# Kernel optimization log

Measured on AMD Instinct MI355X. Metric: run time of the kernel, lower is better.

Reference implementation:

```python
import jax, jax.numpy as jnp
import numpy as np

B, N, E, D = 32, 512, 2048, 128
N_STEPS = 3


def setup_inputs() -> dict:
    key = jax.random.key(0)
    ks = jax.random.split(key, 16)
    s = 0.05
    return {
        "prop_state": jax.random.normal(ks[0], (B, N, D), jnp.float32),
        "edge_states": jax.random.normal(ks[1], (B, E, D), jnp.float32),
        "A": jax.random.uniform(ks[2], (B, N, E), jnp.float32) / E,
        "tem_features": jax.random.normal(ks[3], (B, 64), jnp.float32),
        "link_W": jax.random.normal(ks[4], (D, D), jnp.float32) * s,
        "link_b": jnp.zeros((D,), jnp.float32),
        "reset_W": jax.random.normal(ks[5], (2 * D, D), jnp.float32) * s,
        "reset_b": jnp.zeros((D,), jnp.float32),
        "update_W": jax.random.normal(ks[6], (2 * D, D), jnp.float32) * s,
        "update_b": jnp.zeros((D,), jnp.float32),
        "trans_W": jax.random.normal(ks[7], (2 * D, D), jnp.float32) * s,
        "trans_b": jnp.zeros((D,), jnp.float32),
        "att_W1": jax.random.normal(ks[8], (D, D), jnp.float32) * s,
        "att_b1": jnp.zeros((D,), jnp.float32),
        "att_W2": jax.random.normal(ks[9], (D, 1), jnp.float32) * s,
        "att_b2": jnp.zeros((1,), jnp.float32),
        "out_W": jax.random.normal(ks[10], (D, D), jnp.float32) * s,
        "out_b": jnp.zeros((D,), jnp.float32),
    }


def reference(prop_state, edge_states, A, tem_features,
              link_W, link_b, reset_W, reset_b, update_W, update_b,
              trans_W, trans_b, att_W1, att_b1, att_W2, att_b2, out_W, out_b):
    init_node = prop_state
    init_edge = edge_states
    for _ in range(N_STEPS):
        edge_states = edge_states @ link_W + link_b              # [B,E,D]
        a_cur = jnp.einsum('bne,bed->bnd', A, edge_states)       # [B,N,D]
        a = jnp.concatenate([a_cur, prop_state], axis=2)         # [B,N,2D]
        r = jax.nn.sigmoid(a @ reset_W + reset_b)
        z = jax.nn.sigmoid(a @ update_W + update_b)
        joined = jnp.concatenate([a_cur, r * prop_state], axis=2)
        h_hat = jnp.tanh(joined @ trans_W + trans_b)
        prop_state = (1.0 - z) * prop_state + z * h_hat
    # attention pooling
    atten = jnp.tanh(prop_state @ att_W1 + att_b1) @ att_W2 + att_b2   # [B,N,1]
    Aw = jax.nn.softmax(jnp.transpose(atten, (0, 2, 1)), axis=2)       # [B,1,N]
    out = jnp.tanh(prop_state @ out_W + out_b)                         # [B,N,D]
    mul = jnp.einsum('bqn,bnd->bqd', Aw, out)                          # [B,1,D]
    graph_out = jnp.tanh(jnp.squeeze(mul, axis=1))                     # [B,D]
    # residual block: mean over concatenated node+edge initial states
    feat = jnp.concatenate([init_node, init_edge], axis=1)             # [B,N+E,D]
    residual = jnp.mean(feat, axis=1)                                  # [B,D]
    res = jax.nn.relu(graph_out + residual)
    return res, mul, edge_states
```

## Files before the change

kernel.cpp:

```cpp
#include <hip/hip_runtime.h>
#include <hip/hip_bf16.h>


typedef unsigned short u16;
typedef __attribute__((ext_vector_type(4))) float f32x4;
typedef __attribute__((ext_vector_type(8))) short bf16x8;

#define DI static __device__ __forceinline__

DI u16 f2bf(float f) {
    unsigned u = __builtin_bit_cast(unsigned, f);
    return (u16)((u + 0x7fffu + ((u >> 16) & 1u)) >> 16);
}

DI bf16x8 cvt8(float4 a, float4 b) {
    u16 tmp[8] = {f2bf(a.x), f2bf(a.y), f2bf(a.z), f2bf(a.w),
                  f2bf(b.x), f2bf(b.y), f2bf(b.z), f2bf(b.w)};
    return *(const bf16x8*)tmp;
}

DI int imgIdx(int k, int n) {
    return (((k >> 5) * 128 + n) * 4 + (((k >> 3) & 3) ^ ((n >> 1) & 3))) * 8 + (k & 7);
}
DI bf16x8 wfragG(const u16* __restrict__ img, int kc, int tt, int l15, int quad) {
    return *(const bf16x8*)&img[(((kc * 128 + tt * 16 + l15) * 4) + (quad ^ ((l15 >> 1) & 3))) * 8];
}

#define MFMA16(a, b, c) __builtin_amdgcn_mfma_f32_16x16x32_bf16(a, b, c, 0, 0, 0)

__global__ __launch_bounds__(256) void k_prep1(
    const float* __restrict__ linkW, const float* __restrict__ resetW,
    const float* __restrict__ updateW, const float* __restrict__ transW,
    const float* __restrict__ attW1, const float* __restrict__ outW,
    float* __restrict__ W2, u16* __restrict__ linkImg, u16* __restrict__ WrImg,
    u16* __restrict__ WzImg, u16* __restrict__ WhImg, u16* __restrict__ attW1Img,
    u16* __restrict__ outWImg)
{
    int blk = blockIdx.x, t = threadIdx.x;
    if (blk < 256) {
        int idx = blk * 256 + t;
        int out = idx >> 2, q = idx & 3;
        int r = out >> 7, c = out & 127;
        const float* ar = linkW + r * 128 + q * 32;
        float acc = 0.f;
#pragma unroll
        for (int k = 0; k < 32; k++) acc += ar[k] * linkW[(q * 32 + k) * 128 + c];
        acc += __shfl_xor(acc, 1);
        acc += __shfl_xor(acc, 2);
        if (q == 0) W2[out] = acc;
    } else {
        const float* src; u16* dst; int base;
        if (blk < 260)      { src = resetW;  dst = WrImg;    base = 256; }
        else if (blk < 264) { src = updateW; dst = WzImg;    base = 260; }
        else if (blk < 268) { src = transW;  dst = WhImg;    base = 264; }
        else if (blk < 270) { src = linkW;   dst = linkImg;  base = 268; }
        else if (blk < 272) { src = attW1;   dst = attW1Img; base = 270; }
        else                { src = outW;    dst = outWImg;  base = 272; }
        int off = (blk - base) * 8192;
        for (int i = 0; i < 32; i++) {
            int e = off + t + i * 256;
            int k = e >> 7, n = e & 127;
            dst[imgIdx(k, n)] = f2bf(src[e]);
        }
    }
}

__global__ __launch_bounds__(256) void k_prep2(
    const float* __restrict__ linkW, const float* __restrict__ linkb,
    const float* __restrict__ W2, u16* __restrict__ W3Img, float* __restrict__ ebias)
{
    int blk = blockIdx.x, t = threadIdx.x;
    if (blk < 256) {
        int idx = blk * 256 + t;
        int out = idx >> 2, q = idx & 3;
        int r = out >> 7, c = out & 127;
        const float* ar = W2 + r * 128 + q * 32;
        float acc = 0.f;
#pragma unroll
        for (int k = 0; k < 32; k++) acc += ar[k] * linkW[(q * 32 + k) * 128 + c];
        acc += __shfl_xor(acc, 1);
        acc += __shfl_xor(acc, 2);
        if (q == 0) W3Img[imgIdx(r, c)] = f2bf(acc);
    } else if (t < 128) {
        float acc = linkb[t];
#pragma unroll 8
        for (int k = 0; k < 128; k++) acc += linkb[k] * (W2[k * 128 + t] + linkW[k * 128 + t]);
        ebias[t] = acc;
    }
}

__global__ __launch_bounds__(256) void k_te(
    const float* __restrict__ E0, u16* __restrict__ Eswz, float* __restrict__ resid)
{
    __shared__ alignas(16) u16 sT[4096];
    __shared__ float sCol[128];
    int t = threadIdx.x, kc = blockIdx.x, b = blockIdx.y;
    const float* Eb = E0 + (size_t)b * 262144 + (size_t)kc * 32 * 128;
    if (t < 128) sCol[t] = 0.f;
    float part[4] = {0.f, 0.f, 0.f, 0.f};
    int ncol = (t & 31) * 4;
    for (int i = 0; i < 4; i++) {
        int f4i = t + i * 256;
        int k5 = f4i >> 5;
        float4 v = *(const float4*)&Eb[k5 * 128 + ncol];
        int g = k5 >> 3, o = k5 & 7;
        float vv[4] = {v.x, v.y, v.z, v.w};
#pragma unroll
        for (int j = 0; j < 4; j++) {
            int n = ncol + j;
            sT[(n * 4 + (g ^ ((n >> 1) & 3))) * 8 + o] = f2bf(vv[j]);
            part[j] += vv[j];
        }
    }
    __syncthreads();
#pragma unroll
    for (int j = 0; j < 4; j++) atomicAdd(&sCol[ncol + j], part[j]);
    u16* dst = Eswz + (size_t)b * 262144 + (size_t)kc * 4096;
    ((uint4*)dst)[t] = ((const uint4*)sT)[t];
    ((uint4*)dst)[t + 256] = ((const uint4*)sT)[t + 256];
    __syncthreads();
    if (t < 128) atomicAdd(&resid[b * 128 + t], sCol[t]);
}

__global__ __launch_bounds__(256, 3) void k_g0(
    const float* __restrict__ A, const u16* __restrict__ Eswz,
    u16* __restrict__ aOut, float* __restrict__ rowsum)
{
    __shared__ float sAcc[4][16][128];
    __shared__ float sRs[4][16];
    int t = threadIdx.x, wid = t >> 6, lane = t & 63, l15 = lane & 15, quad = lane >> 4;
    int bx = blockIdx.x;
    int g = bx >> 8, rmod = bx & 255;
    int b = (rmod & 7) + 8 * g;
    int s = (rmod >> 3) & 31;
    size_t r0 = (size_t)b * 512 + (size_t)s * 16;
    const u16* Eb = Eswz + (size_t)b * 262144;
    const float* Ar = A + (r0 + l15) * 2048;
    int kbase = wid * 16;

    f32x4 acc[8];
#pragma unroll
    for (int i = 0; i < 8; i++) acc[i] = (f32x4){0.f, 0.f, 0.f, 0.f};
    float rsum = 0.f;

    float4 xc = *(const float4*)&Ar[kbase * 32 + quad * 8];
    float4 yc = *(const float4*)&Ar[kbase * 32 + quad * 8 + 4];
    bf16x8 bc[8];
#pragma unroll
    for (int tt = 0; tt < 8; tt++) bc[tt] = wfragG(Eb, kbase, tt, l15, quad);

    for (int kc = 0; kc < 16; kc++) {
        int kg = kbase + kc;
        float4 xn, yn; bf16x8 bn[8];
        if (kc < 15) {
            xn = *(const float4*)&Ar[(kg + 1) * 32 + quad * 8];
            yn = *(const float4*)&Ar[(kg + 1) * 32 + quad * 8 + 4];
#pragma unroll
            for (int tt = 0; tt < 8; tt++) bn[tt] = wfragG(Eb, kg + 1, tt, l15, quad);
        }
        rsum += xc.x + xc.y + xc.z + xc.w + yc.x + yc.y + yc.z + yc.w;
        bf16x8 af = cvt8(xc, yc);
#pragma unroll
        for (int tt = 0; tt < 8; tt++) acc[tt] = MFMA16(af, bc[tt], acc[tt]);
        if (kc < 15) {
            xc = xn; yc = yn;
#pragma unroll
            for (int tt = 0; tt < 8; tt++) bc[tt] = bn[tt];
        }
    }
    rsum += __shfl_xor(rsum, 16);
    rsum += __shfl_xor(rsum, 32);
    if (quad == 0) sRs[wid][l15] = rsum;
#pragma unroll
    for (int tt = 0; tt < 8; tt++)
#pragma unroll
        for (int r = 0; r < 4; r++)
            sAcc[wid][quad * 4 + r][tt * 16 + l15] = acc[tt][r];
    __syncthreads();
    {
        int row = t >> 4, c8 = (t & 15) * 8;
        u16 o[8];
#pragma unroll
        for (int j = 0; j < 8; j++) {
            float v = sAcc[0][row][c8 + j] + sAcc[1][row][c8 + j] +
                      sAcc[2][row][c8 + j] + sAcc[3][row][c8 + j];
            o[j] = f2bf(v);
        }
        *(uint4*)&aOut[(r0 + row) * 128 + c8] = *(const uint4*)o;
    }
    if (t < 16)
        rowsum[r0 + t] = sRs[0][t] + sRs[1][t] + sRs[2][t] + sRs[3][t];
}

__global__ __launch_bounds__(256) void k_steps(
    const u16* __restrict__ aBuf0, const float* __restrict__ p0,
    const float* __restrict__ rowsum,
    const u16* __restrict__ linkImg, const u16* __restrict__ WrImg,
    const u16* __restrict__ WzImg, const u16* __restrict__ WhImg,
    const u16* __restrict__ attW1Img, const u16* __restrict__ outWImg,
    const float* __restrict__ link_b, const float* __restrict__ reset_b,
    const float* __restrict__ update_b, const float* __restrict__ trans_b,
    const float* __restrict__ att_b1, const float* __restrict__ att_W2,
    const float* __restrict__ att_b2, const float* __restrict__ out_b,
    float* __restrict__ atten, float* __restrict__ outPool,
    float* __restrict__ resid)
{
    __shared__ alignas(16) u16 sA[16 * 136], sRP[16 * 136], sP[16 * 136];
    __shared__ float sRed[16];
    int t = threadIdx.x, wave = t >> 6, lane = t & 63, l15 = lane & 15, quad = lane >> 4;
    size_t r0 = (size_t)blockIdx.x * 16;
    int bb = blockIdx.x >> 5;
    int ttA = wave * 2, ttB = wave * 2 + 1;
    int colA = ttA * 16 + l15, colB = ttB * 16 + l15;
    if (t < 16) sRed[t] = 0.f;

    bf16x8 aF[4], pF[4];
#pragma unroll
    for (int kc = 0; kc < 4; kc++) {
        aF[kc] = *(const bf16x8*)&aBuf0[(r0 + l15) * 128 + kc * 32 + quad * 8];
        float4 x = *(const float4*)&p0[(r0 + l15) * 128 + kc * 32 + quad * 8];
        float4 y = *(const float4*)&p0[(r0 + l15) * 128 + kc * 32 + quad * 8 + 4];
        pF[kc] = cvt8(x, y);
    }
    f32x4 pS[2];
#pragma unroll
    for (int j = 0; j < 2; j++)
#pragma unroll
        for (int r = 0; r < 4; r++)
            pS[j][r] = p0[(r0 + quad * 4 + r) * 128 + (wave * 2 + j) * 16 + l15];
    {
        float s0 = pS[0][0] + pS[0][1] + pS[0][2] + pS[0][3];
        float s1 = pS[1][0] + pS[1][1] + pS[1][2] + pS[1][3];
        s0 += __shfl_xor(s0, 16); s0 += __shfl_xor(s0, 32);
        s1 += __shfl_xor(s1, 16); s1 += __shfl_xor(s1, 32);
        if (quad == 0) {
            atomicAdd(&resid[bb * 128 + colA], s0);
            atomicAdd(&resid[bb * 128 + colB], s1);
        }
    }
    float sv[4];
#pragma unroll
    for (int r = 0; r < 4; r++) sv[r] = rowsum[r0 + quad * 4 + r];
    float lbA = link_b[colA], lbB = link_b[colB];
    float rbA = reset_b[colA], rbB = reset_b[colB];
    float ubA = update_b[colA], ubB = update_b[colB];
    float tbA = trans_b[colA], tbB = trans_b[colB];

    f32x4 zero4 = {0.f, 0.f, 0.f, 0.f};
    for (int step = 0; step < 3; step++) {
        f32x4 cA = zero4, cB = zero4;
#pragma unroll
        for (int kc = 0; kc < 4; kc++) {
            cA = MFMA16(aF[kc], wfragG(linkImg, kc, ttA, l15, quad), cA);
            cB = MFMA16(aF[kc], wfragG(linkImg, kc, ttB, l15, quad), cB);
        }
#pragma unroll
        for (int r = 0; r < 4; r++) {
            sA[(quad * 4 + r) * 136 + colA] = f2bf(cA[r] + sv[r] * lbA);
            sA[(quad * 4 + r) * 136 + colB] = f2bf(cB[r] + sv[r] * lbB);
        }
        __syncthreads();
#pragma unroll
        for (int kc = 0; kc < 4; kc++)
            aF[kc] = *(const bf16x8*)&sA[l15 * 136 + kc * 32 + quad * 8];
        f32x4 rA = zero4, rB = zero4, zA = zero4, zB = zero4;
#pragma unroll
        for (int kc = 0; kc < 8; kc++) {
            bf16x8 af = (kc < 4) ? aF[kc] : pF[kc - 4];
            rA = MFMA16(af, wfragG(WrImg, kc, ttA, l15, quad), rA);
            rB = MFMA16(af, wfragG(WrImg, kc, ttB, l15, quad), rB);
            zA = MFMA16(af, wfragG(WzImg, kc, ttA, l15, quad), zA);
            zB = MFMA16(af, wfragG(WzImg, kc, ttB, l15, quad), zB);
        }
#pragma unroll
        for (int r = 0; r < 4; r++) {
            float rvA = 1.f / (1.f + __expf(-(rA[r] + rbA)));
            float rvB = 1.f / (1.f + __expf(-(rB[r] + rbB)));
            zA[r] = 1.f / (1.f + __expf(-(zA[r] + ubA)));
            zB[r] = 1.f / (1.f + __expf(-(zB[r] + ubB)));
            sRP[(quad * 4 + r) * 136 + colA] = f2bf(rvA * pS[0][r]);
            sRP[(quad * 4 + r) * 136 + colB] = f2bf(rvB * pS[1][r]);
        }
        __syncthreads();
        bf16x8 rpF[4];
#pragma unroll
        for (int kc = 0; kc < 4; kc++)
            rpF[kc] = *(const bf16x8*)&sRP[l15 * 136 + kc * 32 + quad * 8];
        f32x4 hA = zero4, hB = zero4;
#pragma unroll
        for (int kc = 0; kc < 8; kc++) {
            bf16x8 af = (kc < 4) ? aF[kc] : rpF[kc - 4];
            hA = MFMA16(af, wfragG(WhImg, kc, ttA, l15, quad), hA);
            hB = MFMA16(af, wfragG(WhImg, kc, ttB, l15, quad), hB);
        }
#pragma unroll
        for (int r = 0; r < 4; r++) {
            float h1 = tanhf(hA[r] + tbA), h2 = tanhf(hB[r] + tbB);
            pS[0][r] = (1.f - zA[r]) * pS[0][r] + zA[r] * h1;
            pS[1][r] = (1.f - zB[r]) * pS[1][r] + zB[r] * h2;
            sP[(quad * 4 + r) * 136 + colA] = f2bf(pS[0][r]);
            sP[(quad * 4 + r) * 136 + colB] = f2bf(pS[1][r]);
        }
        __syncthreads();
#pragma unroll
        for (int kc = 0; kc < 4; kc++)
            pF[kc] = *(const bf16x8*)&sP[l15 * 136 + kc * 32 + quad * 8];
    }
    f32x4 atA = zero4, atB = zero4, oA = zero4, oB = zero4;
#pragma unroll
    for (int kc = 0; kc < 4; kc++) {
        atA = MFMA16(pF[kc], wfragG(attW1Img, kc, ttA, l15, quad), atA);
        atB = MFMA16(pF[kc], wfragG(attW1Img, kc, ttB, l15, quad), atB);
        oA  = MFMA16(pF[kc], wfragG(outWImg,  kc, ttA, l15, quad), oA);
        oB  = MFMA16(pF[kc], wfragG(outWImg,  kc, ttB, l15, quad), oB);
    }
    float b1A = att_b1[colA], b1B = att_b1[colB];
    float w2A = att_W2[colA], w2B = att_W2[colB];
    float obA = out_b[colA],  obB = out_b[colB];
    float pr[4];
#pragma unroll
    for (int r = 0; r < 4; r++) {
        pr[r] = tanhf(atA[r] + b1A) * w2A + tanhf(atB[r] + b1B) * w2B;
        outPool[(r0 + quad * 4 + r) * 128 + colA] = tanhf(oA[r] + obA);
        outPool[(r0 + quad * 4 + r) * 128 + colB] = tanhf(oB[r] + obB);
    }
#pragma unroll
    for (int r = 0; r < 4; r++) {
        float v = pr[r];
        v += __shfl_xor(v, 1); v += __shfl_xor(v, 2);
        v += __shfl_xor(v, 4); v += __shfl_xor(v, 8);
        if (l15 == 0) atomicAdd(&sRed[quad * 4 + r], v);
    }
    __syncthreads();
    if (t < 16) atten[r0 + t] = sRed[t] + att_b2[0];
}

__global__ __launch_bounds__(64) void k_eout(
    const float* __restrict__ E0, const u16* __restrict__ W3Img,
    const float* __restrict__ ebias, float* __restrict__ Eout)
{
    int t = threadIdx.x, l15 = t & 15, quad = t >> 4;
    size_t r0 = (size_t)blockIdx.x * 16;
    bf16x8 eF[4];
#pragma unroll
    for (int kc = 0; kc < 4; kc++) {
        float4 x = *(const float4*)&E0[(r0 + l15) * 128 + kc * 32 + quad * 8];
        float4 y = *(const float4*)&E0[(r0 + l15) * 128 + kc * 32 + quad * 8 + 4];
        eF[kc] = cvt8(x, y);
    }
    f32x4 acc[8];
#pragma unroll
    for (int i = 0; i < 8; i++) acc[i] = (f32x4){0.f, 0.f, 0.f, 0.f};
    {
        bf16x8 wc[8], wn[8];
#pragma unroll
        for (int tt = 0; tt < 8; tt++) wc[tt] = wfragG(W3Img, 0, tt, l15, quad);
#pragma unroll
        for (int kc = 0; kc < 4; kc++) {
            if (kc < 3)
#pragma unroll
                for (int tt = 0; tt < 8; tt++) wn[tt] = wfragG(W3Img, kc + 1, tt, l15, quad);
#pragma unroll
            for (int tt = 0; tt < 8; tt++) acc[tt] = MFMA16(eF[kc], wc[tt], acc[tt]);
            if (kc < 3)
#pragma unroll
                for (int tt = 0; tt < 8; tt++) wc[tt] = wn[tt];
        }
    }
#pragma unroll
    for (int tt = 0; tt < 8; tt++) {
        int col = tt * 16 + l15; float eb = ebias[col];
#pragma unroll
        for (int r = 0; r < 4; r++)
            Eout[(r0 + quad * 4 + r) * 128 + col] = acc[tt][r] + eb;
    }
}

__global__ __launch_bounds__(512) void k_fin(
    const float* __restrict__ atten, const float* __restrict__ outPool,
    const float* __restrict__ resid,
    float* __restrict__ outRes, float* __restrict__ outMul)
{
    __shared__ float swv[512];
    __shared__ float sred[512];
    __shared__ float sacc[4][128];
    int t = threadIdx.x, b = blockIdx.x;
    float a = atten[b * 512 + t];
    sred[t] = a; __syncthreads();
    for (int s = 256; s > 0; s >>= 1) { if (t < s) sred[t] = fmaxf(sred[t], sred[t + s]); __syncthreads(); }
    float mx = sred[0]; __syncthreads();
    float e = __expf(a - mx);
    swv[t] = e; sred[t] = e; __syncthreads();
    for (int s = 256; s > 0; s >>= 1) { if (t < s) sred[t] += sred[t + s]; __syncthreads(); }
    float Z = sred[0]; __syncthreads();
    int col = t & 127, q = t >> 7;
    const float* op = outPool + ((size_t)b * 512 + q * 128) * 128 + col;
    float accM = 0.f;
    for (int n = 0; n < 128; n++) accM += swv[q * 128 + n] * op[(size_t)n * 128];
    sacc[q][col] = accM;
    __syncthreads();
    if (t < 128) {
        float mulv = (sacc[0][t] + sacc[1][t] + sacc[2][t] + sacc[3][t]) / Z;
        float rv = resid[b * 128 + t] * (1.f / 2560.f);
        outMul[b * 128 + t] = mulv;
        outRes[b * 128 + t] = fmaxf(0.f, tanhf(mulv) + rv);
    }
}

extern "C" void kernel_launch(void* const* d_in, const int* in_sizes, int n_in,
                              void* d_out, int out_size, void* d_ws, size_t ws_size,
                              hipStream_t stream)
{
    const float* prop0  = (const float*)d_in[0];
    const float* edge0  = (const float*)d_in[1];
    const float* Amat   = (const float*)d_in[2];
    const float* linkW  = (const float*)d_in[4];
    const float* linkb  = (const float*)d_in[5];
    const float* resetW = (const float*)d_in[6];
    const float* resetb = (const float*)d_in[7];
    const float* updateW= (const float*)d_in[8];
    const float* updateb= (const float*)d_in[9];
    const float* transW = (const float*)d_in[10];
    const float* transb = (const float*)d_in[11];
    const float* attW1  = (const float*)d_in[12];
    const float* attb1  = (const float*)d_in[13];
    const float* attW2  = (const float*)d_in[14];
    const float* attb2  = (const float*)d_in[15];
    const float* outW   = (const float*)d_in[16];
    const float* outb   = (const float*)d_in[17];

    char* w = (char*)d_ws;
    u16*   ws_a_bf    = (u16*)(w);
    float* ws_rowsum  = (float*)(w + 4194304);
    float* ws_atten   = (float*)(w + 4259840);
    float* ws_resid   = (float*)(w + 4325376);
    float* ws_W2      = (float*)(w + 4341760);
    float* ws_ebias   = (float*)(w + 4407296);
    u16*   ws_linkImg = (u16*)(w + 4407808);
    u16*   ws_W3Img   = (u16*)(w + 4440576);
    u16*   ws_WrImg   = (u16*)(w + 4473344);
    u16*   ws_WzImg   = (u16*)(w + 4538880);
    u16*   ws_WhImg   = (u16*)(w + 4604416);
    u16*   ws_attW1Img= (u16*)(w + 4669952);
    u16*   ws_outWImg = (u16*)(w + 4702720);

    float* out_res  = (float*)d_out;
    float* out_mul  = out_res + 4096;
    float* out_edge = out_res + 8192;
    u16*   Eswz     = (u16*)out_edge;
    float* outPool  = out_edge + 4194304;

    hipMemsetAsync(ws_resid, 0, 32 * 128 * sizeof(float), stream);
    k_prep1<<<274, 256, 0, stream>>>(linkW, resetW, updateW, transW, attW1, outW,
                                     ws_W2, ws_linkImg, ws_WrImg, ws_WzImg, ws_WhImg,
                                     ws_attW1Img, ws_outWImg);
    k_prep2<<<257, 256, 0, stream>>>(linkW, linkb, ws_W2, ws_W3Img, ws_ebias);
    k_te<<<dim3(64, 32), 256, 0, stream>>>(edge0, Eswz, ws_resid);
    k_g0<<<1024, 256, 0, stream>>>(Amat, Eswz, ws_a_bf, ws_rowsum);
    k_steps<<<1024, 256, 0, stream>>>(ws_a_bf, prop0, ws_rowsum,
                                      ws_linkImg, ws_WrImg, ws_WzImg, ws_WhImg,
                                      ws_attW1Img, ws_outWImg,
                                      linkb, resetb, updateb, transb,
                                      attb1, attW2, attb2, outb,
                                      ws_atten, outPool, ws_resid);
    k_fin<<<32, 512, 0, stream>>>(ws_atten, outPool, ws_resid, out_res, out_mul);
    k_eout<<<4096, 64, 0, stream>>>(edge0, ws_W3Img, ws_ebias, out_edge);
}
```

Measured before the change: 374.2 us.

## Fuse A@E GEMM kernel into GRU steps kernel, keep aggregate in LDS

Merges k_g0 (the A·E aggregation GEMM producing bf16 a and row sums) into k_steps, so each block computes its 16-row aggregate and row sums into shared memory and then runs the three GRU steps directly. This removes one kernel launch and the global round trip through the bf16 aggregate and rowsum workspace buffers. The fused kernel keeps __launch_bounds__(256,3) and combines both shared-memory footprints, which may lower occupancy for the step phase. It also adds an unroll pragma to the pooling loop in k_fin.

```diff
diff --git a/kernel.cpp b/kernel.cpp
--- a/kernel.cpp
+++ b/kernel.cpp
@@ -122,79 +122,9 @@
     if (t < 128) atomicAdd(&resid[b * 128 + t], sCol[t]);
 }
 
-__global__ __launch_bounds__(256, 3) void k_g0(
+__global__ __launch_bounds__(256, 3) void k_main(
     const float* __restrict__ A, const u16* __restrict__ Eswz,
-    u16* __restrict__ aOut, float* __restrict__ rowsum)
-{
-    __shared__ float sAcc[4][16][128];
-    __shared__ float sRs[4][16];
-    int t = threadIdx.x, wid = t >> 6, lane = t & 63, l15 = lane & 15, quad = lane >> 4;
-    int bx = blockIdx.x;
-    int g = bx >> 8, rmod = bx & 255;
-    int b = (rmod & 7) + 8 * g;
-    int s = (rmod >> 3) & 31;
-    size_t r0 = (size_t)b * 512 + (size_t)s * 16;
-    const u16* Eb = Eswz + (size_t)b * 262144;
-    const float* Ar = A + (r0 + l15) * 2048;
-    int kbase = wid * 16;
-
-    f32x4 acc[8];
-#pragma unroll
-    for (int i = 0; i < 8; i++) acc[i] = (f32x4){0.f, 0.f, 0.f, 0.f};
-    float rsum = 0.f;
-
-    float4 xc = *(const float4*)&Ar[kbase * 32 + quad * 8];
-    float4 yc = *(const float4*)&Ar[kbase * 32 + quad * 8 + 4];
-    bf16x8 bc[8];
-#pragma unroll
-    for (int tt = 0; tt < 8; tt++) bc[tt] = wfragG(Eb, kbase, tt, l15, quad);
-
-    for (int kc = 0; kc < 16; kc++) {
-        int kg = kbase + kc;
-        float4 xn, yn; bf16x8 bn[8];
-        if (kc < 15) {
-            xn = *(const float4*)&Ar[(kg + 1) * 32 + quad * 8];
-            yn = *(const float4*)&Ar[(kg + 1) * 32 + quad * 8 + 4];
-#pragma unroll
-            for (int tt = 0; tt < 8; tt++) bn[tt] = wfragG(Eb, kg + 1, tt, l15, quad);
-        }
-        rsum += xc.x + xc.y + xc.z + xc.w + yc.x + yc.y + yc.z + yc.w;
-        bf16x8 af = cvt8(xc, yc);
-#pragma unroll
-        for (int tt = 0; tt < 8; tt++) acc[tt] = MFMA16(af, bc[tt], acc[tt]);
-        if (kc < 15) {
-            xc = xn; yc = yn;
-#pragma unroll
-            for (int tt = 0; tt < 8; tt++) bc[tt] = bn[tt];
-        }
-    }
-    rsum += __shfl_xor(rsum, 16);
-    rsum += __shfl_xor(rsum, 32);
-    if (quad == 0) sRs[wid][l15] = rsum;
-#pragma unroll
-    for (int tt = 0; tt < 8; tt++)
-#pragma unroll
-        for (int r = 0; r < 4; r++)
-            sAcc[wid][quad * 4 + r][tt * 16 + l15] = acc[tt][r];
-    __syncthreads();
-    {
-        int row = t >> 4, c8 = (t & 15) * 8;
-        u16 o[8];
-#pragma unroll
-        for (int j = 0; j < 8; j++) {
-            float v = sAcc[0][row][c8 + j] + sAcc[1][row][c8 + j] +
-                      sAcc[2][row][c8 + j] + sAcc[3][row][c8 + j];
-            o[j] = f2bf(v);
-        }
-        *(uint4*)&aOut[(r0 + row) * 128 + c8] = *(const uint4*)o;
-    }
-    if (t < 16)
-        rowsum[r0 + t] = sRs[0][t] + sRs[1][t] + sRs[2][t] + sRs[3][t];
-}
-
-__global__ __launch_bounds__(256) void k_steps(
-    const u16* __restrict__ aBuf0, const float* __restrict__ p0,
-    const float* __restrict__ rowsum,
+    const float* __restrict__ p0,
     const u16* __restrict__ linkImg, const u16* __restrict__ WrImg,
     const u16* __restrict__ WzImg, const u16* __restrict__ WhImg,
     const u16* __restrict__ attW1Img, const u16* __restrict__ outWImg,
@@ -205,19 +135,84 @@
     float* __restrict__ atten, float* __restrict__ outPool,
     float* __restrict__ resid)
 {
+    __shared__ float sAcc[4][16][128];
+    __shared__ float sRs[4][16];
     __shared__ alignas(16) u16 sA[16 * 136], sRP[16 * 136], sP[16 * 136];
     __shared__ float sRed[16];
-    int t = threadIdx.x, wave = t >> 6, lane = t & 63, l15 = lane & 15, quad = lane >> 4;
-    size_t r0 = (size_t)blockIdx.x * 16;
-    int bb = blockIdx.x >> 5;
+
+    int t = threadIdx.x, wid = t >> 6, lane = t & 63, l15 = lane & 15, quad = lane >> 4;
+    int bx = blockIdx.x;
+    int g = bx >> 8, rmod = bx & 255;
+    int b = (rmod & 7) + 8 * g;
+    int s = (rmod >> 3) & 31;
+    size_t r0 = (size_t)b * 512 + (size_t)s * 16;
+
+    {
+        const u16* Eb = Eswz + (size_t)b * 262144;
+        const float* Ar = A + (r0 + l15) * 2048;
+        int kbase = wid * 16;
+
+        f32x4 acc[8];
+#pragma unroll
+        for (int i = 0; i < 8; i++) acc[i] = (f32x4){0.f, 0.f, 0.f, 0.f};
+        float rsum = 0.f;
+
+        float4 xc = *(const float4*)&Ar[kbase * 32 + quad * 8];
+        float4 yc = *(const float4*)&Ar[kbase * 32 + quad * 8 + 4];
+        bf16x8 bc[8];
+#pragma unroll
+        for (int tt = 0; tt < 8; tt++) bc[tt] = wfragG(Eb, kbase, tt, l15, quad);
+
+        for (int kc = 0; kc < 16; kc++) {
+            int kg = kbase + kc;
+            float4 xn, yn; bf16x8 bn[8];
+            if (kc < 15) {
+                xn = *(const float4*)&Ar[(kg + 1) * 32 + quad * 8];
+                yn = *(const float4*)&Ar[(kg + 1) * 32 + quad * 8 + 4];
+#pragma unroll
+                for (int tt = 0; tt < 8; tt++) bn[tt] = wfragG(Eb, kg + 1, tt, l15, quad);
+            }
+            rsum += xc.x + xc.y + xc.z + xc.w + yc.x + yc.y + yc.z + yc.w;
+            bf16x8 af = cvt8(xc, yc);
+#pragma unroll
+            for (int tt = 0; tt < 8; tt++) acc[tt] = MFMA16(af, bc[tt], acc[tt]);
+            if (kc < 15) {
+                xc = xn; yc = yn;
+#pragma unroll
+                for (int tt = 0; tt < 8; tt++) bc[tt] = bn[tt];
+            }
+        }
+        rsum += __shfl_xor(rsum, 16);
+        rsum += __shfl_xor(rsum, 32);
+        if (quad == 0) sRs[wid][l15] = rsum;
+#pragma unroll
+        for (int tt = 0; tt < 8; tt++)
+#pragma unroll
+            for (int r = 0; r < 4; r++)
+                sAcc[wid][quad * 4 + r][tt * 16 + l15] = acc[tt][r];
+    }
+    __syncthreads();
+    {
+        int row = t >> 4, c8 = (t & 15) * 8;
+#pragma unroll
+        for (int j = 0; j < 8; j++) {
+            float v = sAcc[0][row][c8 + j] + sAcc[1][row][c8 + j] +
+                      sAcc[2][row][c8 + j] + sAcc[3][row][c8 + j];
+            sA[row * 136 + c8 + j] = f2bf(v);
+        }
+    }
+    if (t < 16) sRed[t] = sRs[0][t] + sRs[1][t] + sRs[2][t] + sRs[3][t];
+    __syncthreads();
+
+    int wave = wid;
+    int bb = b;
     int ttA = wave * 2, ttB = wave * 2 + 1;
     int colA = ttA * 16 + l15, colB = ttB * 16 + l15;
-    if (t < 16) sRed[t] = 0.f;
 
     bf16x8 aF[4], pF[4];
 #pragma unroll
     for (int kc = 0; kc < 4; kc++) {
-        aF[kc] = *(const bf16x8*)&aBuf0[(r0 + l15) * 128 + kc * 32 + quad * 8];
+        aF[kc] = *(const bf16x8*)&sA[l15 * 136 + kc * 32 + quad * 8];
         float4 x = *(const float4*)&p0[(r0 + l15) * 128 + kc * 32 + quad * 8];
         float4 y = *(const float4*)&p0[(r0 + l15) * 128 + kc * 32 + quad * 8 + 4];
         pF[kc] = cvt8(x, y);
@@ -240,11 +235,14 @@
     }
     float sv[4];
 #pragma unroll
-    for (int r = 0; r < 4; r++) sv[r] = rowsum[r0 + quad * 4 + r];
+    for (int r = 0; r < 4; r++) sv[r] = sRed[quad * 4 + r];
     float lbA = link_b[colA], lbB = link_b[colB];
     float rbA = reset_b[colA], rbB = reset_b[colB];
     float ubA = update_b[colA], ubB = update_b[colB];
     float tbA = trans_b[colA], tbB = trans_b[colB];
+
+    __syncthreads();
+    if (t < 16) sRed[t] = 0.f;
 
     f32x4 zero4 = {0.f, 0.f, 0.f, 0.f};
     for (int step = 0; step < 3; step++) {
@@ -396,6 +394,7 @@
     int col = t & 127, q = t >> 7;
     const float* op = outPool + ((size_t)b * 512 + q * 128) * 128 + col;
     float accM = 0.f;
+#pragma unroll 8
     for (int n = 0; n < 128; n++) accM += swv[q * 128 + n] * op[(size_t)n * 128];
     sacc[q][col] = accM;
     __syncthreads();
@@ -443,6 +442,7 @@
     u16*   ws_WhImg   = (u16*)(w + 4604416);
     u16*   ws_attW1Img= (u16*)(w + 4669952);
     u16*   ws_outWImg = (u16*)(w + 4702720);
+    (void)ws_a_bf; (void)ws_rowsum;
 
     float* out_res  = (float*)d_out;
     float* out_mul  = out_res + 4096;
@@ -456,13 +456,12 @@
                                      ws_attW1Img, ws_outWImg);
     k_prep2<<<257, 256, 0, stream>>>(linkW, linkb, ws_W2, ws_W3Img, ws_ebias);
     k_te<<<dim3(64, 32), 256, 0, stream>>>(edge0, Eswz, ws_resid);
-    k_g0<<<1024, 256, 0, stream>>>(Amat, Eswz, ws_a_bf, ws_rowsum);
-    k_steps<<<1024, 256, 0, stream>>>(ws_a_bf, prop0, ws_rowsum,
-                                      ws_linkImg, ws_WrImg, ws_WzImg, ws_WhImg,
-                                      ws_attW1Img, ws_outWImg,
-                                      linkb, resetb, updateb, transb,
-                                      attb1, attW2, attb2, outb,
-                                      ws_atten, outPool, ws_resid);
+    k_main<<<1024, 256, 0, stream>>>(Amat, Eswz, prop0,
+                                     ws_linkImg, ws_WrImg, ws_WzImg, ws_WhImg,
+                                     ws_attW1Img, ws_outWImg,
+                                     linkb, resetb, updateb, transb,
+                                     attb1, attW2, attb2, outb,
+                                     ws_atten, outPool, ws_resid);
     k_fin<<<32, 512, 0, stream>>>(ws_atten, outPool, ws_resid, out_res, out_mul);
     k_eout<<<4096, 64, 0, stream>>>(edge0, ws_W3Img, ws_ebias, out_edge);
 }
```

After: 489.7 us. +30.9%, slower.
